# Kernel optimization log

Measured on AMD Instinct MI355X. Metric: run time of the kernel, lower is better.

The kernel has to match this reference:

```python
import jax, jax.numpy as jnp
import numpy as np

N_NODES = 200000  # graph size
D = 128           # feature dim == out_size
N1 = 81920        # layer-1 node set size
B = 8192          # batch size
K = 10            # num_sample neighbors


def setup_inputs() -> dict:
    key = jax.random.key(0)
    k = jax.random.split(key, 7)
    raw_features = jax.random.normal(k[0], (N_NODES, D), dtype=jnp.float32)
    # xavier-like scale for weights [out, 2*in]
    W1 = jax.random.normal(k[1], (D, 2 * D), dtype=jnp.float32) * (1.0 / np.sqrt(2 * D))
    W2 = jax.random.normal(k[2], (D, 2 * D), dtype=jnp.float32) * (1.0 / np.sqrt(2 * D))
    layer1_nodes = jax.random.randint(k[3], (N1,), 0, N_NODES)
    neigh0_idx = jax.random.randint(k[4], (N1, K), 0, N_NODES)
    map_batch = jax.random.randint(k[5], (B,), 0, N1)
    neigh1_idx = jax.random.randint(k[6], (B, K), 0, N1)
    return {
        "raw_features": raw_features,
        "W1": W1,
        "W2": W2,
        "layer1_nodes": layer1_nodes,
        "neigh0_idx": neigh0_idx,
        "map_batch": map_batch,
        "neigh1_idx": neigh1_idx,
    }


def _sage_layer(self_feats, agg_feats, W):
    # combined = cat([self, agg], dim=1); relu(W @ combined.T).T == relu(combined @ W.T)
    combined = jnp.concatenate([self_feats, agg_feats], axis=1)
    return jax.nn.relu(combined @ W.T)


def reference(raw_features, W1, W2, layer1_nodes, neigh0_idx, map_batch, neigh1_idx):
    # Layer 1: aggregate raw features over K sampled neighbors (MEAN), gcn=False
    agg0 = jnp.mean(raw_features[neigh0_idx], axis=1)        # [N1, D]
    self0 = raw_features[layer1_nodes]                        # [N1, D]
    h1 = _sage_layer(self0, agg0, W1)                         # [N1, D]
    # Layer 2: aggregate layer-1 embeddings for the batch nodes
    agg1 = jnp.mean(h1[neigh1_idx], axis=1)                   # [B, D]
    self1 = h1[map_batch]                                     # [B, D]
    h2 = _sage_layer(self1, agg1, W2)                         # [B, D]
    return h2
```

## Files before the change

### kernel.cpp

```cpp
#include <hip/hip_runtime.h>
#include <stdint.h>

#define D 128
#define K_NEI 10
#define TILE_M 64

typedef __bf16 bf16x8 __attribute__((ext_vector_type(8)));
typedef float f32x4 __attribute__((ext_vector_type(4)));

__device__ __forceinline__ uint32_t f2bf(float f) {
    union { float f; uint32_t u; } v; v.f = f;
    uint32_t u = v.u;
    return (u + 0x7FFFu + ((u >> 16) & 1u)) >> 16;
}
__device__ __forceinline__ float bf2f(uint32_t h) {
    union { uint32_t u; float f; } v; v.u = h << 16; return v.f;
}
__device__ __forceinline__ uint32_t pack2(float a, float b) {
    return f2bf(a) | (f2bf(b) << 16);
}
__device__ __forceinline__ bf16x8 u4_as_bf16x8(uint4 u) {
    union { uint4 u; bf16x8 b; } v; v.u = u; return v.b;
}
__device__ __forceinline__ uint2 cvt4(f32x4 v) {
    union { __bf16 b[4]; uint2 u; } o;
    o.b[0] = (__bf16)v[0]; o.b[1] = (__bf16)v[1];
    o.b[2] = (__bf16)v[2]; o.b[3] = (__bf16)v[3];
    return o.u;
}

__global__ void convert_Wc(const float* __restrict__ W1, const float* __restrict__ W2,
                           uint16_t* __restrict__ O1, uint16_t* __restrict__ O2)
{
    const float* W = (blockIdx.x < 16) ? W1 : W2;
    uint16_t*    O = (blockIdx.x < 16) ? O1 : O2;
    int t = (blockIdx.x & 15) * 256 + threadIdx.x;
    const float* src = W + (size_t)t * 8;
    f32x4 a = *(const f32x4*)src;
    f32x4 b = *(const f32x4*)(src + 4);
    uint4 o;
    o.x = cvt4(a).x; o.y = cvt4(a).y;
    o.z = cvt4(b).x; o.w = cvt4(b).y;
    *(uint4*)(O + (size_t)t * 8) = o;
}

template <bool SRC_F32>
__global__ void gather_agg(const void* __restrict__ src_,
                           const int* __restrict__ self_idx,
                           const int* __restrict__ neigh_idx,
                           uint16_t* __restrict__ C, int M)
{
    const int t = blockIdx.x * 256 + threadIdx.x;
    const int i = t >> 4;
    const int j = t & 15;
    if (i >= M) return;

    const int2* nrow2 = (const int2*)(neigh_idx + (size_t)i * K_NEI);
    int idx[K_NEI];
    #pragma unroll
    for (int k = 0; k < 5; ++k) {
        int2 p = nrow2[k];
        idx[2 * k] = p.x; idx[2 * k + 1] = p.y;
    }
    const int self = self_idx[i];
    uint16_t* c = C + (size_t)i * 256;

    if (SRC_F32) {
        const float* src = (const float*)src_;
        const float* srow = src + (size_t)self * D;
        f32x4 sv0 = *(const f32x4*)(srow + j * 4);
        f32x4 sv1 = *(const f32x4*)(srow + 64 + j * 4);
        f32x4 s0 = (f32x4){0.f,0.f,0.f,0.f};
        f32x4 s1 = (f32x4){0.f,0.f,0.f,0.f};
        #pragma unroll
        for (int k = 0; k < K_NEI; ++k) {
            const float* r = src + (size_t)idx[k] * D;
            s0 += *(const f32x4*)(r + j * 4);
            s1 += *(const f32x4*)(r + 64 + j * 4);
        }
        *(uint2*)(c + j * 4)       = cvt4(sv0);
        *(uint2*)(c + 64 + j * 4)  = cvt4(sv1);
        *(uint2*)(c + 128 + j * 4) = cvt4(s0 * 0.1f);
        *(uint2*)(c + 192 + j * 4) = cvt4(s1 * 0.1f);
    } else {
        const uint16_t* src = (const uint16_t*)src_;
        uint4 sv = *(const uint4*)(src + (size_t)self * D + j * 8);
        float s0=0,s1=0,s2=0,s3=0,s4=0,s5=0,s6=0,s7=0;
        #pragma unroll
        for (int k = 0; k < K_NEI; ++k) {
            uint4 v = *(const uint4*)(src + (size_t)idx[k] * D + j * 8);
            s0 += bf2f(v.x & 0xFFFFu); s1 += bf2f(v.x >> 16);
            s2 += bf2f(v.y & 0xFFFFu); s3 += bf2f(v.y >> 16);
            s4 += bf2f(v.z & 0xFFFFu); s5 += bf2f(v.z >> 16);
            s6 += bf2f(v.w & 0xFFFFu); s7 += bf2f(v.w >> 16);
        }
        *(uint4*)(c + j * 8) = sv;
        const float inv = 0.1f;
        uint4 o;
        o.x = pack2(s0 * inv, s1 * inv); o.y = pack2(s2 * inv, s3 * inv);
        o.z = pack2(s4 * inv, s5 * inv); o.w = pack2(s6 * inv, s7 * inv);
        *(uint4*)(c + 128 + j * 8) = o;
    }
}

template <bool OUT_F32>
__global__ __launch_bounds__(256)
void gemm_k256(const uint16_t* __restrict__ A,
               const uint16_t* __restrict__ Wc,
               void* __restrict__ out_, int M)
{
    const int tid  = threadIdx.x;
    const int wave = tid >> 6;
    const int lane = tid & 63;
    const int r16  = lane & 15;
    const int q    = lane >> 4;
    const int h    = wave & 1;

    const int nTiles = M >> 4;
    const int stride = gridDim.x * 2;
    int tile = blockIdx.x * 2 + (wave >> 1);
    if (tile >= nTiles) return;

    bf16x8 Wf[4][8];
    {
        const uint16_t* wb = Wc + (size_t)(h * 64 + r16) * 256 + q * 8;
        #pragma unroll
        for (int nt = 0; nt < 4; ++nt)
            #pragma unroll
            for (int ks = 0; ks < 8; ++ks)
                Wf[nt][ks] = *(const bf16x8*)(wb + nt * 16 * 256 + ks * 32);
    }

    uint4 preB[8];
    {
        const uint16_t* row = A + (size_t)(tile * 16 + r16) * 256 + q * 8;
        #pragma unroll
        for (int ks = 0; ks < 8; ++ks) preB[ks] = *(const uint4*)(row + ks * 32);
    }

    while (tile < nTiles) {
        const int nxt = tile + stride;

        bf16x8 a[8];
        #pragma unroll
        for (int ks = 0; ks < 8; ++ks) a[ks] = u4_as_bf16x8(preB[ks]);

        if (nxt < nTiles) {
            const uint16_t* row = A + (size_t)(nxt * 16 + r16) * 256 + q * 8;
            #pragma unroll
            for (int ks = 0; ks < 8; ++ks) preB[ks] = *(const uint4*)(row + ks * 32);
        }

        f32x4 acc[4];
        #pragma unroll
        for (int nt = 0; nt < 4; ++nt) acc[nt] = (f32x4){0.f,0.f,0.f,0.f};

        #pragma unroll
        for (int ks = 0; ks < 8; ++ks)
            #pragma unroll
            for (int nt = 0; nt < 4; ++nt)
                acc[nt] = __builtin_amdgcn_mfma_f32_16x16x32_bf16(Wf[nt][ks], a[ks], acc[nt], 0, 0, 0);

        const size_t row = (size_t)(tile * 16 + r16);
        const int col0 = h * 64 + q * 4;
        #pragma unroll
        for (int nt = 0; nt < 4; ++nt) {
            f32x4 v = acc[nt];
            v[0] = v[0] > 0.f ? v[0] : 0.f;
            v[1] = v[1] > 0.f ? v[1] : 0.f;
            v[2] = v[2] > 0.f ? v[2] : 0.f;
            v[3] = v[3] > 0.f ? v[3] : 0.f;
            if (OUT_F32)
                *(f32x4*)((float*)out_ + row * 128 + col0 + nt * 16) = v;
            else
                *(uint2*)((uint16_t*)out_ + row * 128 + col0 + nt * 16) = cvt4(v);
        }
        tile = nxt;
    }
}

template <bool FEATS_F32, bool OUT_F32>
__global__ void sage_layer(const void* __restrict__ feats_,
                           const float* __restrict__ W,
                           const int* __restrict__ self_idx,
                           const int* __restrict__ neigh_idx,
                           void* __restrict__ out_)
{
    __shared__ __align__(16) uint16_t Alds[TILE_M * 128];
    __shared__ __align__(16) uint16_t Wlds[128 * 128];

    const int tid  = threadIdx.x;
    const int wave = tid >> 6;
    const int lane = tid & 63;
    const int r16  = lane & 15;
    const int q    = lane >> 4;
    const int G    = blockIdx.x * TILE_M;

    const float*    feats_f = (const float*)feats_;
    const uint16_t* feats_b = (const uint16_t*)feats_;

    f32x4 acc[8];
    #pragma unroll
    for (int nt = 0; nt < 8; ++nt) acc[nt] = (f32x4){0.f, 0.f, 0.f, 0.f};

    for (int half = 0; half < 2; ++half) {
        #pragma unroll
        for (int it = 0; it < 8; ++it) {
            int t = it * 256 + tid;
            int j = t >> 4, c = t & 15;
            const float* src = W + (size_t)j * 256 + half * 128 + c * 8;
            f32x4 w0 = *(const f32x4*)(src);
            f32x4 w1 = *(const f32x4*)(src + 4);
            uint4 o;
            o.x = pack2(w0[0], w0[1]); o.y = pack2(w0[2], w0[3]);
            o.z = pack2(w1[0], w1[1]); o.w = pack2(w1[2], w1[3]);
            int cs = c ^ (j & 15);
            *(uint4*)(Wlds + j * 128 + cs * 8) = o;
        }
        if (half == 0) {
            #pragma unroll
            for (int it = 0; it < 4; ++it) {
                int t = it * 256 + tid;
                int n = t >> 4, c = t & 15;
                int node = self_idx[G + n];
                uint4 o;
                if (FEATS_F32) {
                    const float* src = feats_f + (size_t)node * D + c * 8;
                    f32x4 f0 = *(const f32x4*)(src);
                    f32x4 f1 = *(const f32x4*)(src + 4);
                    o.x = pack2(f0[0], f0[1]); o.y = pack2(f0[2], f0[3]);
                    o.z = pack2(f1[0], f1[1]); o.w = pack2(f1[2], f1[3]);
                } else {
                    o = *(const uint4*)(feats_b + (size_t)node * D + c * 8);
                }
                int cs = c ^ (n & 15);
                *(uint4*)(Alds + n * 128 + cs * 8) = o;
            }
        } else {
            #pragma unroll
            for (int it = 0; it < 4; ++it) {
                int t = it * 256 + tid;
                int n = t >> 4, c = t & 15;
                const int* nrow = neigh_idx + (size_t)(G + n) * K_NEI;
                float s0=0,s1=0,s2=0,s3=0,s4=0,s5=0,s6=0,s7=0;
                #pragma unroll
                for (int k = 0; k < K_NEI; ++k) {
                    if (FEATS_F32) {
                        const float* src = feats_f + (size_t)nrow[k] * D + c * 8;
                        f32x4 f0 = *(const f32x4*)(src);
                        f32x4 f1 = *(const f32x4*)(src + 4);
                        s0 += f0[0]; s1 += f0[1]; s2 += f0[2]; s3 += f0[3];
                        s4 += f1[0]; s5 += f1[1]; s6 += f1[2]; s7 += f1[3];
                    } else {
                        uint4 v = *(const uint4*)(feats_b + (size_t)nrow[k] * D + c * 8);
                        s0 += bf2f(v.x & 0xFFFFu); s1 += bf2f(v.x >> 16);
                        s2 += bf2f(v.y & 0xFFFFu); s3 += bf2f(v.y >> 16);
                        s4 += bf2f(v.z & 0xFFFFu); s5 += bf2f(v.z >> 16);
                        s6 += bf2f(v.w & 0xFFFFu); s7 += bf2f(v.w >> 16);
                    }
                }
                const float inv = 0.1f;
                uint4 o;
                o.x = pack2(s0 * inv, s1 * inv);
                o.y = pack2(s2 * inv, s3 * inv);
                o.z = pack2(s4 * inv, s5 * inv);
                o.w = pack2(s6 * inv, s7 * inv);
                int cs = c ^ (n & 15);
                *(uint4*)(Alds + n * 128 + cs * 8) = o;
            }
        }
        __syncthreads();

        #pragma unroll
        for (int ks = 0; ks < 4; ++ks) {
            int cidx = ks * 4 + q;
            bf16x8 a = *(const bf16x8*)(Alds + (wave * 16 + r16) * 128 + ((cidx ^ r16) * 8));
            bf16x8 b[8];
            #pragma unroll
            for (int nt = 0; nt < 8; ++nt) {
                int jj = nt * 16 + r16;
                b[nt] = *(const bf16x8*)(Wlds + jj * 128 + ((cidx ^ r16) * 8));
            }
            #pragma unroll
            for (int nt = 0; nt < 8; ++nt)
                acc[nt] = __builtin_amdgcn_mfma_f32_16x16x32_bf16(a, b[nt], acc[nt], 0, 0, 0);
        }
        __syncthreads();
    }

    const int row_base = G + wave * 16 + q * 4;
    #pragma unroll
    for (int nt = 0; nt < 8; ++nt) {
        int col = nt * 16 + r16;
        #pragma unroll
        for (int r = 0; r < 4; ++r) {
            float v = acc[nt][r];
            v = v > 0.f ? v : 0.f;
            if (OUT_F32) ((float*)out_)[(size_t)(row_base + r) * D + col] = v;
            else ((uint16_t*)out_)[(size_t)(row_base + r) * D + col] = (uint16_t)f2bf(v);
        }
    }
}

extern "C" void kernel_launch(void* const* d_in, const int* in_sizes, int n_in,
                              void* d_out, int out_size, void* d_ws, size_t ws_size,
                              hipStream_t stream) {
    const float* raw = (const float*)d_in[0];
    const float* W1  = (const float*)d_in[1];
    const float* W2  = (const float*)d_in[2];
    const int* layer1_nodes = (const int*)d_in[3];
    const int* neigh0       = (const int*)d_in[4];
    const int* map_batch    = (const int*)d_in[5];
    const int* neigh1       = (const int*)d_in[6];

    const int N1 = in_sizes[3];
    const int B  = in_sizes[5];

    const size_t szC1 = (size_t)N1 * 256 * 2;
    const size_t szH1 = (size_t)N1 * 128 * 2;
    const size_t szC2 = (size_t)B * 256 * 2;
    const size_t szW  = 128 * 256 * 2;
    const size_t need = szC1 + szH1 + szC2 + 2 * szW;

    if (ws_size >= need && (N1 % 16) == 0 && (B % 16) == 0) {
        uint16_t* C1  = (uint16_t*)d_ws;
        uint16_t* h1  = C1 + (size_t)N1 * 256;
        uint16_t* C2  = h1 + (size_t)N1 * 128;
        uint16_t* W1c = C2 + (size_t)B * 256;
        uint16_t* W2c = W1c + 128 * 256;

        convert_Wc<<<32, 256, 0, stream>>>(W1, W2, W1c, W2c);

        gather_agg<true ><<<(N1 * 16 + 255) / 256, 256, 0, stream>>>(raw, layer1_nodes, neigh0, C1, N1);

        int g1 = (N1 / 16 + 1) / 2; if (g1 > 512) g1 = 512;
        gemm_k256<false><<<g1, 256, 0, stream>>>(C1, W1c, h1, N1);

        gather_agg<false><<<(B * 16 + 255) / 256, 256, 0, stream>>>(h1, map_batch, neigh1, C2, B);

        int g2 = (B / 16 + 1) / 2; if (g2 > 512) g2 = 512;
        gemm_k256<true ><<<g2, 256, 0, stream>>>(C2, W2c, d_out, B);
        return;
    }

    uint16_t* h1 = (uint16_t*)d_ws;
    sage_layer<true,  false><<<N1 / TILE_M, 256, 0, stream>>>(raw, W1, layer1_nodes, neigh0, h1);
    sage_layer<false, true ><<<B  / TILE_M, 256, 0, stream>>>(h1,  W2, map_batch,    neigh1, d_out);
}
```

Before: 236.1 us.

## Fuse neighbor gather-mean with MFMA GEMM per layer, fold mean scale into weights

Replaces the separate gather kernel, the intermediate combined bf16 buffer and the GEMM kernel with one fused kernel per layer. Each wave gathers 16 rows' self and neighbor features straight into MFMA operand registers and multiplies by bf16 weights read from global/L2. The 1/K mean factor is folded into the aggregate half of the converted weights. This removes the write and re-read of the C1/C2 buffers and two launches. In exchange, weight fragments are reloaded per tile instead of persisting, the kernel uses more registers, and gather latency is no longer separated from compute.

```diff
diff --git a/kernel.cpp b/kernel.cpp
--- a/kernel.cpp
+++ b/kernel.cpp
@@ -27,6 +27,14 @@
     o.b[0] = (__bf16)v[0]; o.b[1] = (__bf16)v[1];
     o.b[2] = (__bf16)v[2]; o.b[3] = (__bf16)v[3];
     return o.u;
+}
+__device__ __forceinline__ bf16x8 cvt8(f32x4 lo, f32x4 hi) {
+    union { __bf16 b[8]; bf16x8 v; } o;
+    o.b[0] = (__bf16)lo[0]; o.b[1] = (__bf16)lo[1];
+    o.b[2] = (__bf16)lo[2]; o.b[3] = (__bf16)lo[3];
+    o.b[4] = (__bf16)hi[0]; o.b[5] = (__bf16)hi[1];
+    o.b[6] = (__bf16)hi[2]; o.b[7] = (__bf16)hi[3];
+    return o.v;
 }
 
 __global__ void convert_Wc(const float* __restrict__ W1, const float* __restrict__ W2,
@@ -35,147 +43,106 @@
     const float* W = (blockIdx.x < 16) ? W1 : W2;
     uint16_t*    O = (blockIdx.x < 16) ? O1 : O2;
     int t = (blockIdx.x & 15) * 256 + threadIdx.x;
+    const float s = (t & 16) ? 0.1f : 1.0f;
     const float* src = W + (size_t)t * 8;
-    f32x4 a = *(const f32x4*)src;
-    f32x4 b = *(const f32x4*)(src + 4);
-    uint4 o;
-    o.x = cvt4(a).x; o.y = cvt4(a).y;
-    o.z = cvt4(b).x; o.w = cvt4(b).y;
+    f32x4 a = *(const f32x4*)src * s;
+    f32x4 b = *(const f32x4*)(src + 4) * s;
+    uint2 lo = cvt4(a), hi = cvt4(b);
+    uint4 o; o.x = lo.x; o.y = lo.y; o.z = hi.x; o.w = hi.y;
     *(uint4*)(O + (size_t)t * 8) = o;
 }
 
-template <bool SRC_F32>
-__global__ void gather_agg(const void* __restrict__ src_,
-                           const int* __restrict__ self_idx,
-                           const int* __restrict__ neigh_idx,
-                           uint16_t* __restrict__ C, int M)
+template <bool SRC_F32, bool OUT_F32>
+__global__ __launch_bounds__(256)
+void sage_fused(const void* __restrict__ src_,
+                const uint16_t* __restrict__ Wc,
+                const int* __restrict__ self_idx,
+                const int* __restrict__ neigh_idx,
+                void* __restrict__ out_, int M)
 {
-    const int t = blockIdx.x * 256 + threadIdx.x;
-    const int i = t >> 4;
-    const int j = t & 15;
-    if (i >= M) return;
-
-    const int2* nrow2 = (const int2*)(neigh_idx + (size_t)i * K_NEI);
+    const int tid  = threadIdx.x;
+    const int lane = tid & 63;
+    const int r16  = lane & 15;
+    const int q    = lane >> 4;
+    const int g    = blockIdx.x * 64 + (tid >> 6) * 16 + r16;
+
+    const int2* nrow2 = (const int2*)(neigh_idx + (size_t)g * K_NEI);
     int idx[K_NEI];
     #pragma unroll
     for (int k = 0; k < 5; ++k) {
         int2 p = nrow2[k];
         idx[2 * k] = p.x; idx[2 * k + 1] = p.y;
     }
-    const int self = self_idx[i];
-    uint16_t* c = C + (size_t)i * 256;
+    const int self = self_idx[g];
+
+    bf16x8 a[8];
+    f32x4 agg[8];
+    #pragma unroll
+    for (int x = 0; x < 8; ++x) agg[x] = (f32x4){0.f, 0.f, 0.f, 0.f};
 
     if (SRC_F32) {
-        const float* src = (const float*)src_;
-        const float* srow = src + (size_t)self * D;
-        f32x4 sv0 = *(const f32x4*)(srow + j * 4);
-        f32x4 sv1 = *(const f32x4*)(srow + 64 + j * 4);
-        f32x4 s0 = (f32x4){0.f,0.f,0.f,0.f};
-        f32x4 s1 = (f32x4){0.f,0.f,0.f,0.f};
+        const float* src  = (const float*)src_;
+        const float* srow = src + (size_t)self * D + q * 8;
+        #pragma unroll
+        for (int ks = 0; ks < 4; ++ks)
+            a[ks] = cvt8(*(const f32x4*)(srow + ks * 32),
+                         *(const f32x4*)(srow + ks * 32 + 4));
         #pragma unroll
         for (int k = 0; k < K_NEI; ++k) {
-            const float* r = src + (size_t)idx[k] * D;
-            s0 += *(const f32x4*)(r + j * 4);
-            s1 += *(const f32x4*)(r + 64 + j * 4);
-        }
-        *(uint2*)(c + j * 4)       = cvt4(sv0);
-        *(uint2*)(c + 64 + j * 4)  = cvt4(sv1);
-        *(uint2*)(c + 128 + j * 4) = cvt4(s0 * 0.1f);
-        *(uint2*)(c + 192 + j * 4) = cvt4(s1 * 0.1f);
+            const float* r = src + (size_t)idx[k] * D + q * 8;
+            #pragma unroll
+            for (int ks = 0; ks < 4; ++ks) {
+                agg[2 * ks]     += *(const f32x4*)(r + ks * 32);
+                agg[2 * ks + 1] += *(const f32x4*)(r + ks * 32 + 4);
+            }
+        }
     } else {
         const uint16_t* src = (const uint16_t*)src_;
-        uint4 sv = *(const uint4*)(src + (size_t)self * D + j * 8);
-        float s0=0,s1=0,s2=0,s3=0,s4=0,s5=0,s6=0,s7=0;
+        #pragma unroll
+        for (int ks = 0; ks < 4; ++ks)
+            a[ks] = u4_as_bf16x8(*(const uint4*)(src + (size_t)self * D + q * 8 + ks * 32));
         #pragma unroll
         for (int k = 0; k < K_NEI; ++k) {
-            uint4 v = *(const uint4*)(src + (size_t)idx[k] * D + j * 8);
-            s0 += bf2f(v.x & 0xFFFFu); s1 += bf2f(v.x >> 16);
-            s2 += bf2f(v.y & 0xFFFFu); s3 += bf2f(v.y >> 16);
-            s4 += bf2f(v.z & 0xFFFFu); s5 += bf2f(v.z >> 16);
-            s6 += bf2f(v.w & 0xFFFFu); s7 += bf2f(v.w >> 16);
-        }
-        *(uint4*)(c + j * 8) = sv;
-        const float inv = 0.1f;
-        uint4 o;
-        o.x = pack2(s0 * inv, s1 * inv); o.y = pack2(s2 * inv, s3 * inv);
-        o.z = pack2(s4 * inv, s5 * inv); o.w = pack2(s6 * inv, s7 * inv);
-        *(uint4*)(c + 128 + j * 8) = o;
-    }
-}
-
-template <bool OUT_F32>
-__global__ __launch_bounds__(256)
-void gemm_k256(const uint16_t* __restrict__ A,
-               const uint16_t* __restrict__ Wc,
-               void* __restrict__ out_, int M)
-{
-    const int tid  = threadIdx.x;
-    const int wave = tid >> 6;
-    const int lane = tid & 63;
-    const int r16  = lane & 15;
-    const int q    = lane >> 4;
-    const int h    = wave & 1;
-
-    const int nTiles = M >> 4;
-    const int stride = gridDim.x * 2;
-    int tile = blockIdx.x * 2 + (wave >> 1);
-    if (tile >= nTiles) return;
-
-    bf16x8 Wf[4][8];
-    {
-        const uint16_t* wb = Wc + (size_t)(h * 64 + r16) * 256 + q * 8;
-        #pragma unroll
-        for (int nt = 0; nt < 4; ++nt)
-            #pragma unroll
-            for (int ks = 0; ks < 8; ++ks)
-                Wf[nt][ks] = *(const bf16x8*)(wb + nt * 16 * 256 + ks * 32);
-    }
-
-    uint4 preB[8];
-    {
-        const uint16_t* row = A + (size_t)(tile * 16 + r16) * 256 + q * 8;
-        #pragma unroll
-        for (int ks = 0; ks < 8; ++ks) preB[ks] = *(const uint4*)(row + ks * 32);
-    }
-
-    while (tile < nTiles) {
-        const int nxt = tile + stride;
-
-        bf16x8 a[8];
-        #pragma unroll
-        for (int ks = 0; ks < 8; ++ks) a[ks] = u4_as_bf16x8(preB[ks]);
-
-        if (nxt < nTiles) {
-            const uint16_t* row = A + (size_t)(nxt * 16 + r16) * 256 + q * 8;
-            #pragma unroll
-            for (int ks = 0; ks < 8; ++ks) preB[ks] = *(const uint4*)(row + ks * 32);
-        }
-
-        f32x4 acc[4];
-        #pragma unroll
-        for (int nt = 0; nt < 4; ++nt) acc[nt] = (f32x4){0.f,0.f,0.f,0.f};
-
-        #pragma unroll
-        for (int ks = 0; ks < 8; ++ks)
-            #pragma unroll
-            for (int nt = 0; nt < 4; ++nt)
-                acc[nt] = __builtin_amdgcn_mfma_f32_16x16x32_bf16(Wf[nt][ks], a[ks], acc[nt], 0, 0, 0);
-
-        const size_t row = (size_t)(tile * 16 + r16);
-        const int col0 = h * 64 + q * 4;
-        #pragma unroll
-        for (int nt = 0; nt < 4; ++nt) {
-            f32x4 v = acc[nt];
-            v[0] = v[0] > 0.f ? v[0] : 0.f;
-            v[1] = v[1] > 0.f ? v[1] : 0.f;
-            v[2] = v[2] > 0.f ? v[2] : 0.f;
-            v[3] = v[3] > 0.f ? v[3] : 0.f;
-            if (OUT_F32)
-                *(f32x4*)((float*)out_ + row * 128 + col0 + nt * 16) = v;
-            else
-                *(uint2*)((uint16_t*)out_ + row * 128 + col0 + nt * 16) = cvt4(v);
-        }
-        tile = nxt;
+            const uint16_t* r = src + (size_t)idx[k] * D + q * 8;
+            #pragma unroll
+            for (int ks = 0; ks < 4; ++ks) {
+                uint4 v = *(const uint4*)(r + ks * 32);
+                agg[2 * ks]     += (f32x4){bf2f(v.x & 0xFFFFu), bf2f(v.x >> 16),
+                                           bf2f(v.y & 0xFFFFu), bf2f(v.y >> 16)};
+                agg[2 * ks + 1] += (f32x4){bf2f(v.z & 0xFFFFu), bf2f(v.z >> 16),
+                                           bf2f(v.w & 0xFFFFu), bf2f(v.w >> 16)};
+            }
+        }
+    }
+    #pragma unroll
+    for (int ks = 0; ks < 4; ++ks)
+        a[4 + ks] = cvt8(agg[2 * ks], agg[2 * ks + 1]);
+
+    f32x4 acc[8];
+    #pragma unroll
+    for (int nt = 0; nt < 8; ++nt) acc[nt] = (f32x4){0.f, 0.f, 0.f, 0.f};
+
+    const uint16_t* wb = Wc + (size_t)r16 * 256 + q * 8;
+    #pragma unroll
+    for (int nt = 0; nt < 8; ++nt)
+        #pragma unroll
+        for (int ks = 0; ks < 8; ++ks) {
+            bf16x8 w = *(const bf16x8*)(wb + (size_t)nt * 16 * 256 + ks * 32);
+            acc[nt] = __builtin_amdgcn_mfma_f32_16x16x32_bf16(w, a[ks], acc[nt], 0, 0, 0);
+        }
+
+    #pragma unroll
+    for (int nt = 0; nt < 8; ++nt) {
+        f32x4 v = acc[nt];
+        v[0] = v[0] > 0.f ? v[0] : 0.f;
+        v[1] = v[1] > 0.f ? v[1] : 0.f;
+        v[2] = v[2] > 0.f ? v[2] : 0.f;
+        v[3] = v[3] > 0.f ? v[3] : 0.f;
+        const int col = nt * 16 + q * 4;
+        if (OUT_F32)
+            *(f32x4*)((float*)out_ + (size_t)g * D + col) = v;
+        else
+            *(uint2*)((uint16_t*)out_ + (size_t)g * D + col) = cvt4(v);
     }
 }
 
@@ -316,30 +283,20 @@
     const int N1 = in_sizes[3];
     const int B  = in_sizes[5];
 
-    const size_t szC1 = (size_t)N1 * 256 * 2;
     const size_t szH1 = (size_t)N1 * 128 * 2;
-    const size_t szC2 = (size_t)B * 256 * 2;
     const size_t szW  = 128 * 256 * 2;
-    const size_t need = szC1 + szH1 + szC2 + 2 * szW;
-
-    if (ws_size >= need && (N1 % 16) == 0 && (B % 16) == 0) {
-        uint16_t* C1  = (uint16_t*)d_ws;
-        uint16_t* h1  = C1 + (size_t)N1 * 256;
-        uint16_t* C2  = h1 + (size_t)N1 * 128;
-        uint16_t* W1c = C2 + (size_t)B * 256;
+    const size_t need = szH1 + 2 * szW;
+
+    if (ws_size >= need && (N1 % 64) == 0 && (B % 64) == 0) {
+        uint16_t* h1  = (uint16_t*)d_ws;
+        uint16_t* W1c = h1 + (size_t)N1 * 128;
         uint16_t* W2c = W1c + 128 * 256;
 
         convert_Wc<<<32, 256, 0, stream>>>(W1, W2, W1c, W2c);
 
-        gather_agg<true ><<<(N1 * 16 + 255) / 256, 256, 0, stream>>>(raw, layer1_nodes, neigh0, C1, N1);
-
-        int g1 = (N1 / 16 + 1) / 2; if (g1 > 512) g1 = 512;
-        gemm_k256<false><<<g1, 256, 0, stream>>>(C1, W1c, h1, N1);
-
-        gather_agg<false><<<(B * 16 + 255) / 256, 256, 0, stream>>>(h1, map_batch, neigh1, C2, B);
-
-        int g2 = (B / 16 + 1) / 2; if (g2 > 512) g2 = 512;
-        gemm_k256<true ><<<g2, 256, 0, stream>>>(C2, W2c, d_out, B);
+        sage_fused<true,  false><<<N1 / 64, 256, 0, stream>>>(raw, W1c, layer1_nodes, neigh0, h1, N1);
+
+        sage_fused<false, true ><<<B  / 64, 256, 0, stream>>>(h1,  W2c, map_batch,    neigh1, d_out, B);
         return;
     }
 
```

Result: slower. 248.9 us (+5.4%).
